# Kernel tuning notes

Hardware: AMD Instinct MI355X
Metric: run time of the kernel (lower is better)

The kernel has to match this reference:

```python
import jax, jax.numpy as jnp
import numpy as np

N, E, L, D, ED, M = 100000, 1600000, 4, 64, 16, 128
BN_EPS = 1e-5


def _bn(x, w, b):
    # BatchNorm1d in training mode: biased batch stats over the node dim
    m = x.mean(0)
    v = jnp.mean((x - m) ** 2, axis=0)
    return (x - m) * jax.lax.rsqrt(v + BN_EPS) * w + b


def _leaky(x):
    return jnp.where(x > 0, x, 0.01 * x)  # torch LeakyReLU default slope


def setup_inputs() -> dict:
    key = jax.random.key(0)
    ks = jax.random.split(key, 8)
    s = 0.05
    return {
        "x": jax.random.normal(ks[0], (N, D), jnp.float32),
        "edge_index": jax.random.randint(ks[1], (2, E), 0, N, jnp.int32),
        "edge_attr": jax.random.normal(ks[2], (E, ED), jnp.float32),
        "bn_pre_w": jnp.ones((L, D), jnp.float32),
        "bn_pre_b": jnp.zeros((L, D), jnp.float32),
        "edge_lin_w": jax.random.normal(ks[3], (L, D, ED), jnp.float32) * s,
        "edge_lin_b": jnp.zeros((L, D), jnp.float32),
        "lin1_w": jax.random.normal(ks[4], (L, D, D), jnp.float32) * s,
        "lin1_b": jnp.zeros((L, D), jnp.float32),
        "bn_mid_w": jnp.ones((L, D), jnp.float32),
        "bn_mid_b": jnp.zeros((L, D), jnp.float32),
        "lin2_w": jax.random.normal(ks[5], (L, D, D), jnp.float32) * s,
        "lin2_b": jnp.zeros((L, D), jnp.float32),
        "eps": jnp.zeros((L,), jnp.float32),
        "cls1_w": jax.random.normal(ks[6], (M, D), jnp.float32) * s,
        "cls1_b": jnp.zeros((M,), jnp.float32),
        "cls_bn_w": jnp.ones((M,), jnp.float32),
        "cls_bn_b": jnp.zeros((M,), jnp.float32),
        "cls2_w": jax.random.normal(ks[7], (1, M), jnp.float32) * s,
        "cls2_b": jnp.zeros((1,), jnp.float32),
    }


def reference(x, edge_index, edge_attr, bn_pre_w, bn_pre_b, edge_lin_w, edge_lin_b,
              lin1_w, lin1_b, bn_mid_w, bn_mid_b, lin2_w, lin2_b, eps,
              cls1_w, cls1_b, cls_bn_w, cls_bn_b, cls2_w, cls2_b):
    src, dst = edge_index[0], edge_index[1]
    h = x
    for i in range(L):  # fixed, small layer count
        hn = _bn(h, bn_pre_w[i], bn_pre_b[i])
        hi = hn if i == 0 else _leaky(hn)
        # GINEConv: msg = relu(x_src + Lin(edge_attr)); sum-aggregate at dst
        e = edge_attr @ edge_lin_w[i].T + edge_lin_b[i]            # [E, D]
        msg = jax.nn.relu(hi[src] + e)                              # gather [E, D]
        aggr = jax.ops.segment_sum(msg, dst, num_segments=N)        # scatter [N, D]
        z = (1.0 + eps[i]) * hi + aggr
        # nn: Linear -> BN -> LeakyReLU -> Linear
        z = z @ lin1_w[i].T + lin1_b[i]
        z = _leaky(_bn(z, bn_mid_w[i], bn_mid_b[i]))
        z = z @ lin2_w[i].T + lin2_b[i]
        h = z if i == 0 else h + z  # residual (skipped on first layer)
    y = _leaky(_bn(h @ cls1_w.T + cls1_b, cls_bn_w, cls_bn_b))
    y = y @ cls2_w.T + cls2_b
    return y.reshape(-1)  # torch.flatten -> [N]
```

## Files before the change

kernel.cpp:

```cpp
#include <hip/hip_runtime.h>
#include <hip/hip_bf16.h>
#include <hip/hip_fp16.h>

constexpr int GN = 100000;
constexpr int GE = 1600000;
constexpr float FN = 100000.0f;
constexpr float BN_EPS = 1e-5f;

constexpr int SB = 512;
constexpr int TILE = (GE + SB - 1) / SB;

typedef __attribute__((ext_vector_type(8))) short bf16x8;
typedef __attribute__((ext_vector_type(4))) float f32x4;

__device__ __forceinline__ unsigned packbf2(float a, float b) {
    __hip_bfloat162 h = __float22bfloat162_rn(float2{a, b});
    union { __hip_bfloat162 h2; unsigned u; } cv;
    cv.h2 = h;
    return cv.u;
}

__device__ __forceinline__ unsigned packh2(float a, float b) {
    __half2 h = __floats2half2_rn(a, b);
    union { __half2 h2; unsigned u; } cv;
    cv.h2 = h;
    return cv.u;
}

__device__ __forceinline__ __half2 u2h(unsigned u) {
    union { unsigned u; __half2 h2; } cv;
    cv.u = u;
    return cv.h2;
}

__device__ __forceinline__ unsigned short bf16rn(float f) {
    unsigned u = __builtin_bit_cast(unsigned, f);
    unsigned r = (u + 0x7FFF + ((u >> 16) & 1)) >> 16;
    return (unsigned short)r;
}

__device__ __forceinline__ float bfu16(unsigned short u) {
    return __builtin_bit_cast(float, (unsigned)u << 16);
}

__device__ __forceinline__ int permb(int b) { return ((b & 7) << 6) | (b >> 3); }


__global__ __launch_bounds__(256) void h1_kernel(const int* __restrict__ dst,
                                                 int* __restrict__ hist1,
                                                 const float* __restrict__ l1w,
                                                 const float* __restrict__ l2w,
                                                 const float* __restrict__ c1w,
                                                 unsigned short* __restrict__ wb,
                                                 float* __restrict__ zeroBuf) {
    __shared__ int cnt[256];
    int b = blockIdx.x, t = threadIdx.x;
    if (b == 0 && t < 128) zeroBuf[t] = 0.f;
    cnt[t] = 0;
    __syncthreads();
    int e0 = b * TILE, e1 = min(e0 + TILE, GE);
    for (int i = e0 + t; i < e1; i += 256)
        atomicAdd(&cnt[dst[i] & 255], 1);
    __syncthreads();
    hist1[t * SB + permb(b)] = cnt[t];
    for (int i = b * 256 + t; i < 40960; i += SB * 256) {
        float v;
        if (i < 16384) v = l1w[i];
        else if (i < 32768) v = l2w[i - 16384];
        else v = c1w[i - 32768];
        wb[i] = bf16rn(v);
    }
}

__global__ __launch_bounds__(256) void s1_kernel(int* __restrict__ hist,
                                                 int* __restrict__ binTot) {
    int bin = blockIdx.x, t = threadIdx.x;
    int v0 = hist[bin * SB + 2 * t], v1 = hist[bin * SB + 2 * t + 1];
    int s = v0 + v1;
    int lane = t & 63, w = t >> 6;
    int incl = s;
    for (int o = 1; o < 64; o <<= 1) {
        int u = __shfl_up(incl, o, 64);
        if (lane >= o) incl += u;
    }
    __shared__ int ws_[4];
    if (lane == 63) ws_[w] = incl;
    __syncthreads();
    int wb = 0;
#pragma unroll
    for (int k = 0; k < 4; ++k)
        if (k < w) wb += ws_[k];
    int ex = wb + incl - s;
    hist[bin * SB + 2 * t] = ex;
    hist[bin * SB + 2 * t + 1] = ex + v0;
    if (t == 255) binTot[bin] = ex + s;
}

__global__ __launch_bounds__(256) void s2_kernel(int* __restrict__ a, int n) {
    int t = threadIdx.x;
    int v0 = (2 * t < n) ? a[2 * t] : 0;
    int v1 = (2 * t + 1 < n) ? a[2 * t + 1] : 0;
    int s = v0 + v1;
    int lane = t & 63, w = t >> 6;
    int incl = s;
    for (int o = 1; o < 64; o <<= 1) {
        int u = __shfl_up(incl, o, 64);
        if (lane >= o) incl += u;
    }
    __shared__ int ws_[4];
    if (lane == 63) ws_[w] = incl;
    __syncthreads();
    int wb = 0;
#pragma unroll
    for (int k = 0; k < 4; ++k)
        if (k < w) wb += ws_[k];
    int ex = wb + incl - s;
    if (2 * t < n) a[2 * t] = ex;
    if (2 * t + 1 < n) a[2 * t + 1] = ex + v0;
}

__global__ __launch_bounds__(256) void scat1_kernel(const int* __restrict__ dst,
                                                    const int* __restrict__ hist1,
                                                    const int* __restrict__ binBase1,
                                                    uint2* __restrict__ out) {
    __shared__ int base[256];
    int b = blockIdx.x, t = threadIdx.x;
    base[t] = hist1[t * SB + permb(b)] + binBase1[t];
    __syncthreads();
    int e0 = b * TILE, e1 = min(e0 + TILE, GE);
    for (int i = e0 + t; i < e1; i += 256) {
        int dv = dst[i];
        int pos = atomicAdd(&base[dv & 255], 1);
        uint2 pr;
        pr.x = (unsigned)i;
        pr.y = (unsigned)dv;
        out[pos] = pr;
    }
}

__global__ __launch_bounds__(256) void h2_kernel(const uint2* __restrict__ in,
                                                 int* __restrict__ hist2) {
    __shared__ int cnt[512];
    int b = blockIdx.x, t = threadIdx.x;
    int tp = permb(b);
    cnt[t] = 0;
    cnt[t + 256] = 0;
    __syncthreads();
    int e0 = tp * TILE, e1 = min(e0 + TILE, GE);
    for (int i = e0 + t; i < e1; i += 256)
        atomicAdd(&cnt[in[i].y >> 8], 1);
    __syncthreads();
    hist2[t * SB + tp] = cnt[t];
    hist2[(t + 256) * SB + tp] = cnt[t + 256];
}

__global__ __launch_bounds__(256) void scat2_kernel(const uint2* __restrict__ in,
                                                    const int* __restrict__ hist2,
                                                    const int* __restrict__ binBase2,
                                                    uint2* __restrict__ out) {
    __shared__ int base[512];
    int b = blockIdx.x, t = threadIdx.x;
    int tp = permb(b);
    base[t] = hist2[t * SB + tp] + binBase2[t];
    base[t + 256] = hist2[(t + 256) * SB + tp] + binBase2[t + 256];
    __syncthreads();
    int e0 = tp * TILE, e1 = min(e0 + TILE, GE);
    int lane = t & 63, w = t >> 6;
    unsigned long long below = (1ull << lane) - 1ull;
    if (lane == 63) below = ~0ull >> 1;
    for (int r = e0; r < e1; r += 256) {
        int i = r + t;
        bool valid = (i < e1);
        uint2 el;
        el.x = 0u; el.y = 0u;
        if (valid) el = in[i];
        int bin = (int)(el.y >> 8);
        unsigned long long m = __ballot(valid);
#pragma unroll
        for (int bb = 0; bb < 9; ++bb) {
            unsigned long long bm = __ballot((bin >> bb) & 1);
            m &= ((bin >> bb) & 1) ? bm : ~bm;
        }
        int rank = __popcll(m & below);
        int cntm = __popcll(m);
        bool leader = valid && ((m & below) == 0ull);
#pragma unroll
        for (int ws = 0; ws < 4; ++ws) {
            if (w == ws && valid) {
                int p0 = base[bin];
                if (leader) base[bin] = p0 + cntm;
                out[p0 + rank] = el;
            }
            __syncthreads();
        }
    }
}

__global__ __launch_bounds__(256) void off_kernel(const uint2* __restrict__ sorted,
                                                  int* __restrict__ off) {
    int n = blockIdx.x * 256 + threadIdx.x;
    if (n > GN) return;
    if (n == GN) { off[GN] = GE; return; }
    int lo = 0, hi = GE;
    while (lo < hi) {
        int mid = (lo + hi) >> 1;
        if ((int)sorted[mid].y < n) lo = mid + 1; else hi = mid;
    }
    off[n] = lo;
}

__global__ __launch_bounds__(256) void gather_sorted_kernel(
    const uint2* __restrict__ sorted, const int* __restrict__ src,
    const float4* __restrict__ attr,
    int* __restrict__ srcS, uint2* __restrict__ attrS2) {
    int q = threadIdx.x & 3;
    int row0 = blockIdx.x * 64 + (threadIdx.x >> 2);
    int stride = gridDim.x * 64;
    for (int p = row0; p < GE; p += stride) {
        int eid = (int)sorted[p].x;
        float4 a = attr[(size_t)eid * 4 + q];
        uint2 u;
        u.x = packh2(a.x, a.y);
        u.y = packh2(a.z, a.w);
        attrS2[(size_t)p * 4 + q] = u;
        if (q == 0) srcS[p] = src[eid];
    }
}


__global__ __launch_bounds__(256) void col_stats64(const float* __restrict__ in,
                                                   float* __restrict__ sum,
                                                   float* __restrict__ sq,
                                                   unsigned short* __restrict__ outb) {
    int c = threadIdx.x & 63;
    int lr = threadIdx.x >> 6;
    float s = 0.f, q = 0.f;
    for (int r = blockIdx.x * 4 + lr; r < GN; r += gridDim.x * 4) {
        float v = in[(size_t)r * 64 + c];
        s += v;
        q += v * v;
        outb[(size_t)r * 64 + c] = bf16rn(v);
    }
    __shared__ float S[256];
    S[threadIdx.x] = s;
    __syncthreads();
    if (threadIdx.x < 64) {
        float a = S[threadIdx.x] + S[threadIdx.x + 64] + S[threadIdx.x + 128] + S[threadIdx.x + 192];
        atomicAdd(&sum[threadIdx.x], a);
    }
    __syncthreads();
    S[threadIdx.x] = q;
    __syncthreads();
    if (threadIdx.x < 64) {
        float a = S[threadIdx.x] + S[threadIdx.x + 64] + S[threadIdx.x + 128] + S[threadIdx.x + 192];
        atomicAdd(&sq[threadIdx.x], a);
    }
}


__global__ __launch_bounds__(256) void aggregate_kernel(
    const float* __restrict__ h,
    const unsigned short* __restrict__ hb,
    const float* __restrict__ sumv, const float* __restrict__ sqv,
    const float* __restrict__ bnw, const float* __restrict__ bnb,
    int leaky,
    const int* __restrict__ off,
    const int* __restrict__ srcS,
    const unsigned* __restrict__ attrS,
    const float* __restrict__ Wle, const float* __restrict__ ble,
    const float* __restrict__ epsArr, int layer,
    unsigned short* __restrict__ zb,
    float* __restrict__ zeroBuf) {
    if (blockIdx.x == 0 && threadIdx.x < 128) zeroBuf[threadIdx.x] = 0.f;
    const int d = threadIdx.x & 63;
    const int node = __builtin_amdgcn_readfirstlane(blockIdx.x * 4 + (threadIdx.x >> 6));

    float mean = sumv[d] / FN;
    float var = sqv[d] / FN - mean * mean;
    float cA = rsqrtf(var + BN_EPS) * bnw[d];
    float cB = bnb[d] - mean * cA;

    __half2 wq2[8];
#pragma unroll
    for (int k = 0; k < 8; ++k) {
        float2 t = *(const float2*)(Wle + d * 16 + k * 2);
        wq2[k] = __floats2half2_rn(t.x, t.y);
    }
    float be = ble[d];
    float epsv = 1.0f + epsArr[layer];
    const __half2 hz = __floats2half2_rn(0.f, 0.f);

    int p0 = off[node], p1 = off[node + 1];
    float hv = h[(size_t)node * 64 + d];

    float acc = 0.0f;
    int p = p0;
    int pfull = p0 + ((p1 - p0) & ~7);
    for (; p < pfull; p += 8) {
        int idx[8];
#pragma unroll
        for (int j = 0; j < 8; ++j) idx[j] = srcS[p + j];
        float g[8];
#pragma unroll
        for (int j = 0; j < 8; ++j)
            g[j] = bfu16(hb[(((unsigned)idx[j]) << 6) + d]);
#pragma unroll
        for (int j = 0; j < 8; ++j) {
            const uint4* ar = (const uint4*)(attrS + (size_t)(p + j) * 8);
            uint4 A = ar[0], B = ar[1];
            __half2 e2 = __hfma2(u2h(A.x), wq2[0], hz);
            e2 = __hfma2(u2h(A.y), wq2[1], e2);
            e2 = __hfma2(u2h(A.z), wq2[2], e2);
            e2 = __hfma2(u2h(A.w), wq2[3], e2);
            e2 = __hfma2(u2h(B.x), wq2[4], e2);
            e2 = __hfma2(u2h(B.y), wq2[5], e2);
            e2 = __hfma2(u2h(B.z), wq2[6], e2);
            e2 = __hfma2(u2h(B.w), wq2[7], e2);
            float e = be + __low2float(e2) + __high2float(e2);
            float gg = g[j] * cA + cB;
            if (leaky) gg = fmaxf(gg, 0.01f * gg);
            acc += fmaxf(gg + e, 0.f);
        }
    }
    for (; p < p1; p += 4) {
        int idx[4];
#pragma unroll
        for (int j = 0; j < 4; ++j) {
            int q = p + j;
            if (q > p1 - 1) q = p1 - 1;
            idx[j] = srcS[q];
        }
        float g[4];
#pragma unroll
        for (int j = 0; j < 4; ++j)
            g[j] = bfu16(hb[(((unsigned)idx[j]) << 6) + d]);
#pragma unroll
        for (int j = 0; j < 4; ++j) {
            int q = p + j;
            if (q > p1 - 1) q = p1 - 1;
            const uint4* ar = (const uint4*)(attrS + (size_t)q * 8);
            uint4 A = ar[0], B = ar[1];
            __half2 e2 = __hfma2(u2h(A.x), wq2[0], hz);
            e2 = __hfma2(u2h(A.y), wq2[1], e2);
            e2 = __hfma2(u2h(A.z), wq2[2], e2);
            e2 = __hfma2(u2h(A.w), wq2[3], e2);
            e2 = __hfma2(u2h(B.x), wq2[4], e2);
            e2 = __hfma2(u2h(B.y), wq2[5], e2);
            e2 = __hfma2(u2h(B.z), wq2[6], e2);
            e2 = __hfma2(u2h(B.w), wq2[7], e2);
            float e = be + __low2float(e2) + __high2float(e2);
            float gg = g[j] * cA + cB;
            if (leaky) gg = fmaxf(gg, 0.01f * gg);
            float m = fmaxf(gg + e, 0.f);
            acc += (p + j < p1) ? m : 0.f;
        }
    }
    hv = hv * cA + cB;
    if (leaky) hv = fmaxf(hv, 0.01f * hv);
    zb[(size_t)node * 64 + d] = bf16rn(epsv * hv + acc);
}


template <bool BN_IN, bool ABF16, bool STATS, bool RESID, bool BF16OUT, bool F32OUT>
__global__ __launch_bounds__(256) void gemm_mfma(
    const float* __restrict__ srcf, const unsigned short* __restrict__ srcb, int src_ld,
    const unsigned short* __restrict__ Wb,
    const float* __restrict__ bias,
    float* __restrict__ dst, int dst_ld,
    unsigned short* __restrict__ dstb, int dstb_ld,
    const float* __restrict__ resid,
    const float* __restrict__ statsInSum, const float* __restrict__ statsInSq,
    const float* __restrict__ bnw, const float* __restrict__ bnb,
    float* __restrict__ statsOutSum, float* __restrict__ statsOutSq,
    float* __restrict__ zeroBuf, int zeroN) {
    __shared__ float cA[64], cB[64];
    __shared__ float sS[64], sQ[64];
    int tid = threadIdx.x;
    if (zeroBuf && blockIdx.x == 0 && blockIdx.y == 0 && tid < zeroN) zeroBuf[tid] = 0.f;
    int c0 = blockIdx.y * 64;

    if (BN_IN) {
        if (tid < 64) {
            float m = statsInSum[tid] / FN;
            float v = statsInSq[tid] / FN - m * m;
            float a = rsqrtf(v + BN_EPS) * bnw[tid];
            cA[tid] = a;
            cB[tid] = bnb[tid] - m * a;
        }
        __syncthreads();
    }

    int w = tid >> 6, lane = tid & 63;
    int n16 = lane & 15, quad = lane >> 4;

    bf16x8 bfr[4][2];
#pragma unroll
    for (int t = 0; t < 4; ++t) {
        int col = c0 + t * 16 + n16;
        const unsigned short* bsrc = Wb + (size_t)col * 64 + quad * 8;
#pragma unroll
        for (int kk = 0; kk < 2; ++kk)
            bfr[t][kk] = *(const bf16x8*)(bsrc + kk * 32);
    }

    float ls[4] = {0.f, 0.f, 0.f, 0.f}, lq[4] = {0.f, 0.f, 0.f, 0.f};
    constexpr int NT = (GN + 63) / 64;
    for (int tile = blockIdx.x; tile < NT; tile += gridDim.x) {
        int r0 = tile * 64;
        int arow = r0 + w * 16 + n16;
        int arc = arow < GN ? arow : 0;

        bf16x8 afr[2];
        if (ABF16) {
            const unsigned short* asrc = srcb + (size_t)arc * src_ld + quad * 8;
#pragma unroll
            for (int kk = 0; kk < 2; ++kk)
                afr[kk] = *(const bf16x8*)(asrc + kk * 32);
        } else {
            const float* asrc = srcf + (size_t)arc * src_ld + quad * 8;
#pragma unroll
            for (int kk = 0; kk < 2; ++kk) {
                const float4* p = (const float4*)(asrc + kk * 32);
                float4 x0 = p[0], x1 = p[1];
                float av[8] = {x0.x, x0.y, x0.z, x0.w, x1.x, x1.y, x1.z, x1.w};
                if (BN_IN) {
                    int kb = quad * 8 + kk * 32;
#pragma unroll
                    for (int j = 0; j < 8; ++j) {
                        float t = av[j] * cA[kb + j] + cB[kb + j];
                        av[j] = fmaxf(t, 0.01f * t);
                    }
                }
                uint4 fu;
                fu.x = packbf2(av[0], av[1]); fu.y = packbf2(av[2], av[3]);
                fu.z = packbf2(av[4], av[5]); fu.w = packbf2(av[6], av[7]);
                afr[kk] = __builtin_bit_cast(bf16x8, fu);
            }
        }

        f32x4 acc[4] = {{0.f, 0.f, 0.f, 0.f}, {0.f, 0.f, 0.f, 0.f},
                        {0.f, 0.f, 0.f, 0.f}, {0.f, 0.f, 0.f, 0.f}};
#pragma unroll
        for (int t = 0; t < 4; ++t) {
            acc[t] = __builtin_amdgcn_mfma_f32_16x16x32_bf16(afr[0], bfr[t][0], acc[t], 0, 0, 0);
            acc[t] = __builtin_amdgcn_mfma_f32_16x16x32_bf16(afr[1], bfr[t][1], acc[t], 0, 0, 0);
        }

#pragma unroll
        for (int t = 0; t < 4; ++t) {
            int col = c0 + t * 16 + n16;
            float bv = bias[col];
#pragma unroll
            for (int r = 0; r < 4; ++r) {
                int row = r0 + w * 16 + quad * 4 + r;
                if (row < GN) {
                    float o = acc[t][r] + bv;
                    if (RESID) o += resid[(size_t)row * dst_ld + col];
                    if (F32OUT) dst[(size_t)row * dst_ld + col] = o;
                    if (BF16OUT) dstb[(size_t)row * dstb_ld + col] = bf16rn(o);
                    if (STATS) { ls[t] += o; lq[t] += o * o; }
                }
            }
        }
    }

    if (STATS) {
        if (tid < 64) { sS[tid] = 0.f; sQ[tid] = 0.f; }
        __syncthreads();
#pragma unroll
        for (int t = 0; t < 4; ++t) {
            float s = ls[t], q = lq[t];
            s += __shfl_down(s, 16, 64); s += __shfl_down(s, 32, 64);
            q += __shfl_down(q, 16, 64); q += __shfl_down(q, 32, 64);
            if (lane < 16) {
                atomicAdd(&sS[t * 16 + n16], s);
                atomicAdd(&sQ[t * 16 + n16], q);
            }
        }
        __syncthreads();
        if (tid < 64) {
            atomicAdd(&statsOutSum[c0 + tid], sS[tid]);
            atomicAdd(&statsOutSq[c0 + tid], sQ[tid]);
        }
    }
}


__global__ __launch_bounds__(256) void cls2_kernel(
    const unsigned short* __restrict__ y1b,
    const float* __restrict__ sum, const float* __restrict__ sq,
    const float* __restrict__ bnw, const float* __restrict__ bnb,
    const float* __restrict__ w2, const float* __restrict__ b2,
    float* __restrict__ out) {
    int node = blockIdx.x * 4 + (threadIdx.x >> 6);
    int d = threadIdx.x & 63;
    if (node >= GN) return;
    float partial = 0.f;
#pragma unroll
    for (int hh = 0; hh < 2; ++hh) {
        int c = d + hh * 64;
        float m = sum[c] / FN;
        float var = sq[c] / FN - m * m;
        float a = rsqrtf(var + BN_EPS) * bnw[c];
        float v = bfu16(y1b[(size_t)node * 128 + c]);
        v = v * a + (bnb[c] - m * a);
        v = fmaxf(v, 0.01f * v);
        partial += v * w2[c];
    }
    for (int o = 32; o >= 1; o >>= 1) partial += __shfl_down(partial, o, 64);
    if (d == 0) out[node] = partial + b2[0];
}


extern "C" void kernel_launch(void* const* d_in, const int* in_sizes, int n_in,
                              void* d_out, int out_size, void* d_ws, size_t ws_size,
                              hipStream_t stream) {
    (void)in_sizes; (void)n_in; (void)out_size; (void)ws_size;
    const float* x    = (const float*)d_in[0];
    const int*   ei   = (const int*)d_in[1];
    const float* attr = (const float*)d_in[2];
    const float* bnpw = (const float*)d_in[3];
    const float* bnpb = (const float*)d_in[4];
    const float* elw  = (const float*)d_in[5];
    const float* elb  = (const float*)d_in[6];
    const float* l1w  = (const float*)d_in[7];
    const float* l1b  = (const float*)d_in[8];
    const float* bnmw = (const float*)d_in[9];
    const float* bnmb = (const float*)d_in[10];
    const float* l2w  = (const float*)d_in[11];
    const float* l2b  = (const float*)d_in[12];
    const float* epsA = (const float*)d_in[13];
    const float* c1w  = (const float*)d_in[14];
    const float* c1b  = (const float*)d_in[15];
    const float* cbw  = (const float*)d_in[16];
    const float* cbb  = (const float*)d_in[17];
    const float* c2w  = (const float*)d_in[18];
    const float* c2b  = (const float*)d_in[19];
    const int* srcArr = ei;
    const int* dstArr = ei + GE;

    char* base = (char*)d_ws;
    size_t ofs = 0;
    auto alloc = [&](size_t bytes) {
        void* p = base + ofs;
        ofs = (ofs + bytes + 1023) & ~(size_t)1023;
        return p;
    };
    int* off              = (int*)alloc((size_t)(GN + 1) * 4);
    int* hist1            = (int*)alloc((size_t)256 * SB * 4);
    int* hist2            = (int*)alloc((size_t)512 * SB * 4);
    int* binTot1          = (int*)alloc(512 * 4);
    int* binTot2          = (int*)alloc(512 * 4);
    int* src_sorted       = (int*)alloc((size_t)GE * 4);
    unsigned* attr_sorted = (unsigned*)alloc((size_t)GE * 32);
    unsigned short* wbf   = (unsigned short*)alloc(40960 * 2);
    float* stP0 = (float*)alloc(512);
    float* stP1 = (float*)alloc(512);
    float* stM  = (float*)alloc(512);
    float* stC  = (float*)alloc(1024);
    float* h = (float*)alloc((size_t)GN * 256);
    float* z = (float*)alloc((size_t)GN * 256);
    unsigned short* zb = (unsigned short*)alloc((size_t)GN * 128);
    unsigned short* xb = (unsigned short*)alloc((size_t)GN * 128);
    unsigned short* hb = (unsigned short*)alloc((size_t)GN * 128);
    unsigned short* y1b = (unsigned short*)attr_sorted;
    uint2* pairsA = (uint2*)z;
    uint2* pairsB = (uint2*)((char*)z + (size_t)GE * 8);

    float* stP[2] = {stP0, stP1};

    h1_kernel<<<SB, 256, 0, stream>>>(dstArr, hist1, l1w, l2w, c1w, wbf, stP0);
    s1_kernel<<<256, 256, 0, stream>>>(hist1, binTot1);
    s2_kernel<<<1, 256, 0, stream>>>(binTot1, 256);
    scat1_kernel<<<SB, 256, 0, stream>>>(dstArr, hist1, binTot1, pairsA);
    h2_kernel<<<SB, 256, 0, stream>>>(pairsA, hist2);
    s1_kernel<<<512, 256, 0, stream>>>(hist2, binTot2);
    s2_kernel<<<1, 256, 0, stream>>>(binTot2, 512);
    scat2_kernel<<<SB, 256, 0, stream>>>(pairsA, hist2, binTot2, pairsB);
    off_kernel<<<392, 256, 0, stream>>>(pairsB, off);
    gather_sorted_kernel<<<4096, 256, 0, stream>>>(pairsB, srcArr, (const float4*)attr,
                                                   src_sorted, (uint2*)attr_sorted);

    col_stats64<<<512, 256, 0, stream>>>(x, stP0, stP0 + 64, xb);

    const float* hsrc = x;
    const unsigned short* hbsrc = xb;
    for (int i = 0; i < 4; ++i) {
        float* sIn = stP[i & 1];
        float* sNext = stP[(i + 1) & 1];
        aggregate_kernel<<<25000, 256, 0, stream>>>(
            hsrc, hbsrc, sIn, sIn + 64, bnpw + i * 64, bnpb + i * 64, (i > 0) ? 1 : 0,
            off, src_sorted, attr_sorted, elw + i * 1024, elb + i * 64, epsA, i,
            zb, stM);
        gemm_mfma<false, true, true, false, false, true><<<dim3(782, 1), 256, 0, stream>>>(
            nullptr, zb, 64, wbf + i * 4096, l1b + i * 64, z, 64, nullptr, 0, nullptr,
            nullptr, nullptr, nullptr, nullptr, stM, stM + 64,
            (i == 3) ? stC : sNext, (i == 3) ? 256 : 128);
        if (i == 0)
            gemm_mfma<true, false, true, false, true, true><<<dim3(782, 1), 256, 0, stream>>>(
                z, nullptr, 64, wbf + 16384 + i * 4096, l2b + i * 64, h, 64, hb, 64,
                nullptr, stM, stM + 64, bnmw + i * 64, bnmb + i * 64,
                sNext, sNext + 64, nullptr, 0);
        else if (i < 3)
            gemm_mfma<true, false, true, true, true, true><<<dim3(782, 1), 256, 0, stream>>>(
                z, nullptr, 64, wbf + 16384 + i * 4096, l2b + i * 64, h, 64, hb, 64,
                h, stM, stM + 64, bnmw + i * 64, bnmb + i * 64,
                sNext, sNext + 64, nullptr, 0);
        else
            gemm_mfma<true, false, false, true, true, true><<<dim3(782, 1), 256, 0, stream>>>(
                z, nullptr, 64, wbf + 16384 + i * 4096, l2b + i * 64, h, 64, hb, 64,
                h, stM, stM + 64, bnmw + i * 64, bnmb + i * 64,
                nullptr, nullptr, nullptr, 0);
        hsrc = h;
        hbsrc = hb;
    }

    dim3 gc(391, 2);
    gemm_mfma<false, true, true, false, true, false><<<gc, 256, 0, stream>>>(
        nullptr, hb, 64, wbf + 32768, c1b, nullptr, 128, y1b, 128, nullptr,
        nullptr, nullptr, nullptr, nullptr, stC, stC + 128, nullptr, 0);
    cls2_kernel<<<25000, 256, 0, stream>>>(y1b, stC, stC + 128, cbw, cbb, c2w, c2b,
                                           (float*)d_out);
}
```

Before: 975.1 us.

## Compute per-edge linear projection with MFMA in the aggregate kernel

After: 1.158 ms. 18.8% more time.

```diff
diff --git a/kernel.cpp b/kernel.cpp
--- a/kernel.cpp
+++ b/kernel.cpp
@@ -12,6 +12,7 @@
 
 typedef __attribute__((ext_vector_type(8))) short bf16x8;
 typedef __attribute__((ext_vector_type(4))) float f32x4;
+typedef _Float16 f16x8 __attribute__((ext_vector_type(8)));
 
 __device__ __forceinline__ unsigned packbf2(float a, float b) {
     __hip_bfloat162 h = __float22bfloat162_rn(float2{a, b});
@@ -25,12 +26,6 @@
     union { __half2 h2; unsigned u; } cv;
     cv.h2 = h;
     return cv.u;
-}
-
-__device__ __forceinline__ __half2 u2h(unsigned u) {
-    union { unsigned u; __half2 h2; } cv;
-    cv.u = u;
-    return cv.h2;
 }
 
 __device__ __forceinline__ unsigned short bf16rn(float f) {
@@ -272,92 +267,117 @@
     unsigned short* __restrict__ zb,
     float* __restrict__ zeroBuf) {
     if (blockIdx.x == 0 && threadIdx.x < 128) zeroBuf[threadIdx.x] = 0.f;
-    const int d = threadIdx.x & 63;
+    const int lane = threadIdx.x & 63;
     const int node = __builtin_amdgcn_readfirstlane(blockIdx.x * 4 + (threadIdx.x >> 6));
-
-    float mean = sumv[d] / FN;
-    float var = sqv[d] / FN - mean * mean;
-    float cA = rsqrtf(var + BN_EPS) * bnw[d];
-    float cB = bnb[d] - mean * cA;
-
-    __half2 wq2[8];
-#pragma unroll
-    for (int k = 0; k < 8; ++k) {
-        float2 t = *(const float2*)(Wle + d * 16 + k * 2);
-        wq2[k] = __floats2half2_rn(t.x, t.y);
-    }
-    float be = ble[d];
+    const int col = lane & 15;
+    const int quad = lane >> 4;
+
+    float cA[4], cB[4], bev[4];
+#pragma unroll
+    for (int t = 0; t < 4; ++t) {
+        int f = 16 * t + col;
+        float m = sumv[f] / FN;
+        float v = sqv[f] / FN - m * m;
+        float a = rsqrtf(v + BN_EPS) * bnw[f];
+        cA[t] = a;
+        cB[t] = bnb[f] - m * a;
+        bev[t] = ble[f];
+    }
+    f16x8 bfr[4];
+#pragma unroll
+    for (int t = 0; t < 4; ++t) {
+        f16x8 f8 = {};
+        if (quad < 2) {
+            const float4* wp = (const float4*)(Wle + (16 * t + col) * 16 + quad * 8);
+            float4 w0 = wp[0], w1 = wp[1];
+            f8[0] = (_Float16)w0.x; f8[1] = (_Float16)w0.y;
+            f8[2] = (_Float16)w0.z; f8[3] = (_Float16)w0.w;
+            f8[4] = (_Float16)w1.x; f8[5] = (_Float16)w1.y;
+            f8[6] = (_Float16)w1.z; f8[7] = (_Float16)w1.w;
+        }
+        bfr[t] = f8;
+    }
     float epsv = 1.0f + epsArr[layer];
-    const __half2 hz = __floats2half2_rn(0.f, 0.f);
 
     int p0 = off[node], p1 = off[node + 1];
-    float hv = h[(size_t)node * 64 + d];
-
-    float acc = 0.0f;
+    float acc[4] = {0.f, 0.f, 0.f, 0.f};
+
     int p = p0;
-    int pfull = p0 + ((p1 - p0) & ~7);
-    for (; p < pfull; p += 8) {
-        int idx[8];
-#pragma unroll
-        for (int j = 0; j < 8; ++j) idx[j] = srcS[p + j];
-        float g[8];
-#pragma unroll
-        for (int j = 0; j < 8; ++j)
-            g[j] = bfu16(hb[(((unsigned)idx[j]) << 6) + d]);
-#pragma unroll
-        for (int j = 0; j < 8; ++j) {
-            const uint4* ar = (const uint4*)(attrS + (size_t)(p + j) * 8);
-            uint4 A = ar[0], B = ar[1];
-            __half2 e2 = __hfma2(u2h(A.x), wq2[0], hz);
-            e2 = __hfma2(u2h(A.y), wq2[1], e2);
-            e2 = __hfma2(u2h(A.z), wq2[2], e2);
-            e2 = __hfma2(u2h(A.w), wq2[3], e2);
-            e2 = __hfma2(u2h(B.x), wq2[4], e2);
-            e2 = __hfma2(u2h(B.y), wq2[5], e2);
-            e2 = __hfma2(u2h(B.z), wq2[6], e2);
-            e2 = __hfma2(u2h(B.w), wq2[7], e2);
-            float e = be + __low2float(e2) + __high2float(e2);
-            float gg = g[j] * cA + cB;
-            if (leaky) gg = fmaxf(gg, 0.01f * gg);
-            acc += fmaxf(gg + e, 0.f);
-        }
-    }
-    for (; p < p1; p += 4) {
-        int idx[4];
-#pragma unroll
-        for (int j = 0; j < 4; ++j) {
-            int q = p + j;
+    int pfull = p0 + ((p1 - p0) & ~15);
+    for (; p < pfull; p += 16) {
+        f16x8 afr = {};
+        if (quad < 2)
+            afr = *(const f16x8*)((const char*)attrS + (size_t)(p + col) * 32 + quad * 16);
+        int sb = p + quad * 4;
+        int se0 = srcS[sb], se1 = srcS[sb + 1], se2 = srcS[sb + 2], se3 = srcS[sb + 3];
+        float g[4][4];
+#pragma unroll
+        for (int t = 0; t < 4; ++t) {
+            g[t][0] = bfu16(hb[(((unsigned)se0) << 6) + 16 * t + col]);
+            g[t][1] = bfu16(hb[(((unsigned)se1) << 6) + 16 * t + col]);
+            g[t][2] = bfu16(hb[(((unsigned)se2) << 6) + 16 * t + col]);
+            g[t][3] = bfu16(hb[(((unsigned)se3) << 6) + 16 * t + col]);
+        }
+#pragma unroll
+        for (int t = 0; t < 4; ++t) {
+            f32x4 c = {bev[t], bev[t], bev[t], bev[t]};
+            f32x4 d = __builtin_amdgcn_mfma_f32_16x16x32_f16(afr, bfr[t], c, 0, 0, 0);
+#pragma unroll
+            for (int r = 0; r < 4; ++r) {
+                float gg = g[t][r] * cA[t] + cB[t];
+                if (leaky) gg = fmaxf(gg, 0.01f * gg);
+                acc[t] += fmaxf(gg + d[r], 0.f);
+            }
+        }
+    }
+    if (p < p1) {
+        int arow = p + col;
+        if (arow > p1 - 1) arow = p1 - 1;
+        f16x8 afr = {};
+        if (quad < 2)
+            afr = *(const f16x8*)((const char*)attrS + (size_t)arow * 32 + quad * 16);
+        int se[4];
+#pragma unroll
+        for (int r = 0; r < 4; ++r) {
+            int q = p + quad * 4 + r;
             if (q > p1 - 1) q = p1 - 1;
-            idx[j] = srcS[q];
-        }
-        float g[4];
-#pragma unroll
-        for (int j = 0; j < 4; ++j)
-            g[j] = bfu16(hb[(((unsigned)idx[j]) << 6) + d]);
-#pragma unroll
-        for (int j = 0; j < 4; ++j) {
-            int q = p + j;
-            if (q > p1 - 1) q = p1 - 1;
-            const uint4* ar = (const uint4*)(attrS + (size_t)q * 8);
-            uint4 A = ar[0], B = ar[1];
-            __half2 e2 = __hfma2(u2h(A.x), wq2[0], hz);
-            e2 = __hfma2(u2h(A.y), wq2[1], e2);
-            e2 = __hfma2(u2h(A.z), wq2[2], e2);
-            e2 = __hfma2(u2h(A.w), wq2[3], e2);
-            e2 = __hfma2(u2h(B.x), wq2[4], e2);
-            e2 = __hfma2(u2h(B.y), wq2[5], e2);
-            e2 = __hfma2(u2h(B.z), wq2[6], e2);
-            e2 = __hfma2(u2h(B.w), wq2[7], e2);
-            float e = be + __low2float(e2) + __high2float(e2);
-            float gg = g[j] * cA + cB;
-            if (leaky) gg = fmaxf(gg, 0.01f * gg);
-            float m = fmaxf(gg + e, 0.f);
-            acc += (p + j < p1) ? m : 0.f;
-        }
-    }
-    hv = hv * cA + cB;
-    if (leaky) hv = fmaxf(hv, 0.01f * hv);
-    zb[(size_t)node * 64 + d] = bf16rn(epsv * hv + acc);
+            se[r] = srcS[q];
+        }
+        float g[4][4];
+#pragma unroll
+        for (int t = 0; t < 4; ++t)
+#pragma unroll
+            for (int r = 0; r < 4; ++r)
+                g[t][r] = bfu16(hb[(((unsigned)se[r]) << 6) + 16 * t + col]);
+#pragma unroll
+        for (int t = 0; t < 4; ++t) {
+            f32x4 c = {bev[t], bev[t], bev[t], bev[t]};
+            f32x4 d = __builtin_amdgcn_mfma_f32_16x16x32_f16(afr, bfr[t], c, 0, 0, 0);
+#pragma unroll
+            for (int r = 0; r < 4; ++r) {
+                int q = p + quad * 4 + r;
+                float gg = g[t][r] * cA[t] + cB[t];
+                if (leaky) gg = fmaxf(gg, 0.01f * gg);
+                float m = fmaxf(gg + d[r], 0.f);
+                acc[t] += (q < p1) ? m : 0.f;
+            }
+        }
+    }
+#pragma unroll
+    for (int t = 0; t < 4; ++t) {
+        acc[t] += __shfl_xor(acc[t], 16, 64);
+        acc[t] += __shfl_xor(acc[t], 32, 64);
+    }
+    if (quad == 0) {
+#pragma unroll
+        for (int t = 0; t < 4; ++t) {
+            int f = 16 * t + col;
+            float hv = h[(size_t)node * 64 + f];
+            hv = hv * cA[t] + cB[t];
+            if (leaky) hv = fmaxf(hv, 0.01f * hv);
+            zb[(size_t)node * 64 + f] = bf16rn(epsv * hv + acc[t]);
+        }
+    }
 }
 
 
```
